# Kernel optimization log

Hardware: AMD Instinct MI355X
Metric: run time of the kernel (lower is better)

The kernel has to match this reference:

```python
import jax, jax.numpy as jnp
import numpy as np

B, S, H = 8, 2048, 256
MAX_SEQ = 2048


def get_rotary_matrix(context_window, embedding_dim):
    # Faithful to the llama-from-scratch construction (note the (i-1) quirk):
    # theta_i = 10000 ** (-2*(i-1)/d) for i in [0, d/2)
    half = embedding_dim // 2
    i = jnp.arange(half, dtype=jnp.float32)
    theta = jnp.power(10000.0, -2.0 * (i - 1.0) / embedding_dim)  # [half]
    pos = jnp.arange(context_window, dtype=jnp.float32)  # [S]
    ang = pos[:, None] * theta[None, :]  # [S, half]
    c, s = jnp.cos(ang), jnp.sin(ang)
    R = jnp.zeros((context_window, embedding_dim, embedding_dim), dtype=jnp.float32)
    idx = jnp.arange(half)
    R = R.at[:, 2 * idx, 2 * idx].set(c)
    R = R.at[:, 2 * idx, 2 * idx + 1].set(-s)
    R = R.at[:, 2 * idx + 1, 2 * idx].set(s)
    R = R.at[:, 2 * idx + 1, 2 * idx + 1].set(c)
    return R


def setup_inputs() -> dict:
    key = jax.random.key(0)
    kx, kq, kk, kv = jax.random.split(key, 4)
    scale = 1.0 / np.sqrt(H)
    x = jax.random.normal(kx, (B, S, H), dtype=jnp.float32)
    wq = jax.random.uniform(kq, (H, H), dtype=jnp.float32, minval=-scale, maxval=scale)
    wk = jax.random.uniform(kk, (H, H), dtype=jnp.float32, minval=-scale, maxval=scale)
    wv = jax.random.uniform(kv, (H, H), dtype=jnp.float32, minval=-scale, maxval=scale)
    r = get_rotary_matrix(MAX_SEQ, H)
    return {"x": x, "wq": wq, "wk": wk, "wv": wv, "r": r}


def reference(x, wq, wk, wv, r):
    b, s, h = x.shape
    # nn.Linear(bias=False): y = x @ W.T
    q = jnp.einsum("bsh,oh->bso", x, wq)
    k = jnp.einsum("bsh,oh->bso", x, wk)
    v = jnp.einsum("bsh,oh->bso", x, wv)
    # per-position dense rotary rotation: qr[b,s,:] = q[b,s,:] @ r[s]
    rs = r[:s]
    qr = jnp.einsum("bsh,shk->bsk", q, rs)
    kr = jnp.einsum("bsh,shk->bsk", k, rs)
    attn = jnp.einsum("bqh,bkh->bqk", qr, kr) * (h ** -0.5)  # [B,S,S]
    causal = jnp.tril(jnp.ones((s, s), dtype=bool))
    attn = jnp.where(causal[None, :, :], attn, -jnp.inf)
    attn = jax.nn.softmax(attn, axis=-1)
    out = jnp.einsum("bqk,bkh->bqh", attn, v)
    return out
```

## Files before the change

### kernel.cpp

```cpp
#include <hip/hip_runtime.h>


typedef __bf16 bf16x8 __attribute__((ext_vector_type(8)));
typedef float  f32x4  __attribute__((ext_vector_type(4)));
typedef unsigned short u16x4 __attribute__((ext_vector_type(4)));

#define LOG2E 1.44269504088896340736f
#define LOG2_10000 13.287712379549449f

__device__ __forceinline__ unsigned short f2bf(float f) {
    union { __bf16 h; unsigned short u; } cv;
    cv.h = (__bf16)f;
    return cv.u;
}

__device__ __forceinline__ void gl_lds16(const unsigned short* g, unsigned short* lds) {
    __builtin_amdgcn_global_load_lds(
        (const __attribute__((address_space(1))) unsigned int*)g,
        (__attribute__((address_space(3))) unsigned int*)lds, 16, 0, 0);
}

__global__ __launch_bounds__(256) void build_cs(float2* __restrict__ cs) {
    int id = blockIdx.x * 256 + threadIdx.x;
    int s = id >> 7;
    int i = id & 127;
    float ex = -2.0f * ((float)i - 1.0f) * (1.0f / 256.0f);
    float theta = exp2f(LOG2_10000 * ex);
    float ang = (float)s * theta;
    float sn, c;
    sincosf(ang, &sn, &c);
    cs[id] = make_float2(c, sn);
}

__global__ __launch_bounds__(256, 2) void qkv_rope(
    const float* __restrict__ x,
    const float* __restrict__ wq, const float* __restrict__ wk,
    const float* __restrict__ wv,
    const float2* __restrict__ cs,
    unsigned short* __restrict__ qr, unsigned short* __restrict__ kr,
    unsigned short* __restrict__ vt) {

    __shared__ unsigned short Ash[64 * 64];
    __shared__ unsigned short Bsh[256 * 64];

    const int mt  = blockIdx.x;
    const int sel = blockIdx.y;
    const float* wsel = (sel == 0) ? wq : (sel == 1) ? wk : wv;

    const int tid = threadIdx.x;
    const int w = tid >> 6, l = tid & 63;
    const int lane_m = l & 15, quad = l >> 4;
    const int wm = w >> 1, wn = w & 1;

    f32x4 acc[2][8];
#pragma unroll
    for (int a = 0; a < 2; ++a)
#pragma unroll
        for (int c = 0; c < 8; ++c) acc[a][c] = (f32x4){0.f, 0.f, 0.f, 0.f};

    for (int kc = 0; kc < 4; ++kc) {
        if (kc) __syncthreads();
#pragma unroll
        for (int p = 0; p < 4; ++p) {
            int id = p * 256 + tid;
            int row = id >> 4, f4 = id & 15;
            float4 d = *(const float4*)(x + (size_t)(mt * 64 + row) * 256 + kc * 64 + f4 * 4);
            u16x4 pk = { f2bf(d.x), f2bf(d.y), f2bf(d.z), f2bf(d.w) };
            int k = f4 * 4;
            int idx = row * 64 + ((((k >> 3) ^ (row & 7)) << 3) | (k & 7));
            *(u16x4*)&Ash[idx] = pk;
        }
#pragma unroll
        for (int p = 0; p < 16; ++p) {
            int id = p * 256 + tid;
            int row = id >> 4, f4 = id & 15;
            float4 d = *(const float4*)(wsel + (size_t)row * 256 + kc * 64 + f4 * 4);
            u16x4 pk = { f2bf(d.x), f2bf(d.y), f2bf(d.z), f2bf(d.w) };
            int k = f4 * 4;
            int idx = row * 64 + ((((k >> 3) ^ (row & 7)) << 3) | (k & 7));
            *(u16x4*)&Bsh[idx] = pk;
        }
        __syncthreads();
#pragma unroll
        for (int ks = 0; ks < 2; ++ks) {
            int ch = ks * 4 + quad;
            int r0 = wm * 32 + lane_m;
            bf16x8 a0 = *(const bf16x8*)&Ash[r0 * 64 + ((ch ^ (r0 & 7)) << 3)];
            bf16x8 a1 = *(const bf16x8*)&Ash[(r0 + 16) * 64 + ((ch ^ (r0 & 7)) << 3)];
#pragma unroll
            for (int ct = 0; ct < 8; ++ct) {
                int n = wn * 128 + ct * 16 + lane_m;
                bf16x8 bb = *(const bf16x8*)&Bsh[n * 64 + ((ch ^ (n & 7)) << 3)];
                acc[0][ct] = __builtin_amdgcn_mfma_f32_16x16x32_bf16(a0, bb, acc[0][ct], 0, 0, 0);
                acc[1][ct] = __builtin_amdgcn_mfma_f32_16x16x32_bf16(a1, bb, acc[1][ct], 0, 0, 0);
            }
        }
    }

    if (sel < 2) {
        unsigned short* dst = sel ? kr : qr;
        const float scale = sel ? 1.0f : 0.0625f;
#pragma unroll
        for (int rt = 0; rt < 2; ++rt) {
#pragma unroll
            for (int ct = 0; ct < 8; ++ct) {
                int col = wn * 128 + ct * 16 + lane_m;
                int ii = col >> 1;
                float sgn = (col & 1) ? -1.0f : 1.0f;
                int mbase = mt * 64 + wm * 32 + rt * 16 + quad * 4;
#pragma unroll
                for (int rr = 0; rr < 4; ++rr) {
                    int m = mbase + rr;
                    int spos = m & 2047;
                    float2 csv = cs[spos * 128 + ii];
                    float v = acc[rt][ct][rr];
                    float pr = __shfl_xor(v, 1);
                    float rot = (csv.x * v + sgn * csv.y * pr) * scale;
                    dst[(size_t)m * 256 + col] = f2bf(rot);
                }
            }
        }
    } else {
#pragma unroll
        for (int rt = 0; rt < 2; ++rt) {
#pragma unroll
            for (int ct = 0; ct < 8; ++ct) {
                int col = wn * 128 + ct * 16 + lane_m;
                int mbase = mt * 64 + wm * 32 + rt * 16 + quad * 4;
                u16x4 pk = { f2bf(acc[rt][ct][0]), f2bf(acc[rt][ct][1]),
                             f2bf(acc[rt][ct][2]), f2bf(acc[rt][ct][3]) };
                int bb = mbase >> 11;
                int s0 = mbase & 2047;
                *(u16x4*)&vt[((size_t)bb * 256 + col) * 2048 + s0] = pk;
            }
        }
    }
}

__global__ __launch_bounds__(256, 2) void flash_attn(
    const unsigned short* __restrict__ qr, const unsigned short* __restrict__ kr,
    const unsigned short* __restrict__ vt, float* __restrict__ out) {

    __shared__ unsigned short Ksh[64 * 256];
    __shared__ unsigned short Vsh[256 * 64];
    __shared__ unsigned short Psh[32 * 64];

    const int n = blockIdx.x;
    const int r = (n < 256) ? n : 767 - n;
    const int b = r & 7;
    const int j = 63 - (r >> 3);
    const int q0 = j * 32;

    const int tid = threadIdx.x;
    const int w = tid >> 6, l = tid & 63;
    const int lane_m = l & 15, quad = l >> 4;
    const int qw = w >> 1;
    const int kp = w & 1;

    bf16x8 qf[8];
    {
        const unsigned short* qb =
            qr + ((size_t)(b * 2048 + q0 + qw * 16 + lane_m)) * 256 + quad * 8;
#pragma unroll
        for (int ks = 0; ks < 8; ++ks) qf[ks] = *(const bf16x8*)(qb + ks * 32);
    }

    f32x4 o[16];
#pragma unroll
    for (int t = 0; t < 16; ++t) o[t] = (f32x4){0.f, 0.f, 0.f, 0.f};
    float l_part[4] = {0.f, 0.f, 0.f, 0.f};

    const int nkt = ((q0 + 31) >> 6) + 1;
    const int rmax = q0 + qw * 16 + 15;

    for (int kt = 0; kt < nkt; ++kt) {
        const int kv0 = kt * 64;
        __syncthreads();
#pragma unroll
        for (int p = 0; p < 8; ++p) {
            int rb = (p * 4 + w) * 2;
            int row = rb + (l >> 5);
            int cg = (l & 31) ^ (row & 31);
            gl_lds16(kr + ((size_t)(b * 2048 + kv0 + row)) * 256 + cg * 8, &Ksh[rb * 256]);
        }
#pragma unroll
        for (int p = 0; p < 8; ++p) {
            int hb = (p * 4 + w) * 8;
            int h = hb + (l >> 3);
            int cg = (l & 7) ^ (h & 7);
            gl_lds16(vt + ((size_t)(b * 256 + h)) * 2048 + kv0 + cg * 8, &Vsh[hb * 64]);
        }
        __syncthreads();

        const bool active = (kv0 + 32 * kp) <= rmax;
        if (active) {
            f32x4 sacc[2];
#pragma unroll
            for (int ct = 0; ct < 2; ++ct) sacc[ct] = (f32x4){0.f, 0.f, 0.f, 0.f};
#pragma unroll
            for (int ks = 0; ks < 8; ++ks) {
                bf16x8 a = qf[ks];
#pragma unroll
                for (int ct = 0; ct < 2; ++ct) {
                    int kvr = kp * 32 + ct * 16 + lane_m;
                    bf16x8 bb = *(const bf16x8*)&Ksh[kvr * 256 + (((ks * 4 + quad) ^ (kvr & 31)) << 3)];
                    sacc[ct] = __builtin_amdgcn_mfma_f32_16x16x32_bf16(a, bb, sacc[ct], 0, 0, 0);
                }
            }

            const bool needmask = (kv0 + kp * 32 + 31) > (q0 + qw * 16);
#pragma unroll
            for (int ct = 0; ct < 2; ++ct) {
                int col_l = kp * 32 + ct * 16 + lane_m;
                int col_g = kv0 + col_l;
#pragma unroll
                for (int rr = 0; rr < 4; ++rr) {
                    float e = exp2f(sacc[ct][rr] * LOG2E);
                    if (needmask) {
                        int row_g = q0 + qw * 16 + quad * 4 + rr;
                        if (col_g > row_g) e = 0.0f;
                    }
                    l_part[rr] += e;
                    int row = qw * 16 + quad * 4 + rr;
                    Psh[row * 64 + ((((col_l >> 3) ^ (row & 7)) << 3) | (col_l & 7))] = f2bf(e);
                }
            }

            {
                int prow = qw * 16 + lane_m;
                int pk = kp * 4 + quad;
                bf16x8 a = *(const bf16x8*)&Psh[prow * 64 + ((pk ^ (prow & 7)) << 3)];
#pragma unroll
                for (int ht = 0; ht < 16; ++ht) {
                    int h = ht * 16 + lane_m;
                    bf16x8 bb = *(const bf16x8*)&Vsh[h * 64 + ((pk ^ (h & 7)) << 3)];
                    o[ht] = __builtin_amdgcn_mfma_f32_16x16x32_bf16(a, bb, o[ht], 0, 0, 0);
                }
            }
        }
    }

#pragma unroll
    for (int rr = 0; rr < 4; ++rr) {
        l_part[rr] += __shfl_xor(l_part[rr], 1);
        l_part[rr] += __shfl_xor(l_part[rr], 2);
        l_part[rr] += __shfl_xor(l_part[rr], 4);
        l_part[rr] += __shfl_xor(l_part[rr], 8);
    }

    __syncthreads();
    float* mlbuf = (float*)Vsh;
    float* obuf  = (float*)Ksh;
    if (lane_m == 0) {
#pragma unroll
        for (int rr = 0; rr < 4; ++rr)
            mlbuf[(qw * 2 + kp) * 16 + quad * 4 + rr] = l_part[rr];
    }
    if (kp == 1) {
#pragma unroll
        for (int ht = 0; ht < 16; ++ht)
#pragma unroll
            for (int rr = 0; rr < 4; ++rr)
                obuf[(qw * 16 + quad * 4 + rr) * 256 + ht * 16 + lane_m] = o[ht][rr];
    }
    __syncthreads();
    if (kp == 0) {
        float inv[4];
#pragma unroll
        for (int rr = 0; rr < 4; ++rr)
            inv[rr] = 1.0f / (l_part[rr] + mlbuf[(qw * 2 + 1) * 16 + quad * 4 + rr]);
#pragma unroll
        for (int ht = 0; ht < 16; ++ht) {
#pragma unroll
            for (int rr = 0; rr < 4; ++rr) {
                float val = o[ht][rr] +
                            obuf[(qw * 16 + quad * 4 + rr) * 256 + ht * 16 + lane_m];
                size_t idx = ((size_t)(b * 2048 + q0 + qw * 16 + quad * 4 + rr)) * 256
                             + ht * 16 + lane_m;
                out[idx] = val * inv[rr];
            }
        }
    }
}

extern "C" void kernel_launch(void* const* d_in, const int* in_sizes, int n_in,
                              void* d_out, int out_size, void* d_ws, size_t ws_size,
                              hipStream_t stream) {
    const float* x  = (const float*)d_in[0];
    const float* wq = (const float*)d_in[1];
    const float* wk = (const float*)d_in[2];
    const float* wv = (const float*)d_in[3];
    float* out = (float*)d_out;

    char* ws = (char*)d_ws;
    float2*         cs = (float2*)ws;
    unsigned short* qr = (unsigned short*)(ws + (2u << 20));
    unsigned short* kr = (unsigned short*)(ws + (10u << 20));
    unsigned short* vt = (unsigned short*)(ws + (18u << 20));

    build_cs<<<dim3(1024), dim3(256), 0, stream>>>(cs);
    qkv_rope<<<dim3(256, 3), dim3(256), 0, stream>>>(x, wq, wk, wv, cs, qr, kr, vt);
    flash_attn<<<dim3(512), dim3(256), 0, stream>>>(qr, kr, vt, out);
}
```

Before: 683.6 us.

## Pre-convert weights to bf16 and compute Q/K/V from one x tile per block

New measurement: 698.7 us. 2.2% more time.

```diff
diff --git a/kernel.cpp b/kernel.cpp
--- a/kernel.cpp
+++ b/kernel.cpp
@@ -20,118 +20,128 @@
         (__attribute__((address_space(3))) unsigned int*)lds, 16, 0, 0);
 }
 
-__global__ __launch_bounds__(256) void build_cs(float2* __restrict__ cs) {
-    int id = blockIdx.x * 256 + threadIdx.x;
-    int s = id >> 7;
-    int i = id & 127;
-    float ex = -2.0f * ((float)i - 1.0f) * (1.0f / 256.0f);
-    float theta = exp2f(LOG2_10000 * ex);
-    float ang = (float)s * theta;
-    float sn, c;
-    sincosf(ang, &sn, &c);
-    cs[id] = make_float2(c, sn);
-}
-
-__global__ __launch_bounds__(256, 2) void qkv_rope(
-    const float* __restrict__ x,
+__global__ __launch_bounds__(256) void prep(
     const float* __restrict__ wq, const float* __restrict__ wk,
     const float* __restrict__ wv,
+    float2* __restrict__ cs, unsigned short* __restrict__ wb) {
+    int bid = blockIdx.x;
+    if (bid < 1024) {
+        int id = bid * 256 + threadIdx.x;
+        int s = id >> 7;
+        int i = id & 127;
+        float ex = -2.0f * ((float)i - 1.0f) * (1.0f / 256.0f);
+        float theta = exp2f(LOG2_10000 * ex);
+        float ang = (float)s * theta;
+        float sn, c;
+        sincosf(ang, &sn, &c);
+        cs[id] = make_float2(c, sn);
+    } else {
+        int id = (bid - 1024) * 256 + threadIdx.x;
+        int sel = id >> 14;
+        int off = id & 16383;
+        const float* src = (sel == 0) ? wq : (sel == 1) ? wk : wv;
+        float4 d = ((const float4*)src)[off];
+        u16x4 pk = { f2bf(d.x), f2bf(d.y), f2bf(d.z), f2bf(d.w) };
+        *(u16x4*)&wb[(size_t)sel * 65536 + (size_t)off * 4] = pk;
+    }
+}
+
+__global__ __launch_bounds__(256, 2) void qkv_rope(
+    const float* __restrict__ x, const unsigned short* __restrict__ wb,
     const float2* __restrict__ cs,
     unsigned short* __restrict__ qr, unsigned short* __restrict__ kr,
     unsigned short* __restrict__ vt) {
 
-    __shared__ unsigned short Ash[64 * 64];
+    __shared__ unsigned short Ash[64 * 256];
     __shared__ unsigned short Bsh[256 * 64];
 
     const int mt  = blockIdx.x;
-    const int sel = blockIdx.y;
-    const float* wsel = (sel == 0) ? wq : (sel == 1) ? wk : wv;
-
     const int tid = threadIdx.x;
     const int w = tid >> 6, l = tid & 63;
     const int lane_m = l & 15, quad = l >> 4;
     const int wm = w >> 1, wn = w & 1;
 
-    f32x4 acc[2][8];
-#pragma unroll
-    for (int a = 0; a < 2; ++a)
-#pragma unroll
-        for (int c = 0; c < 8; ++c) acc[a][c] = (f32x4){0.f, 0.f, 0.f, 0.f};
-
-    for (int kc = 0; kc < 4; ++kc) {
-        if (kc) __syncthreads();
-#pragma unroll
-        for (int p = 0; p < 4; ++p) {
-            int id = p * 256 + tid;
-            int row = id >> 4, f4 = id & 15;
-            float4 d = *(const float4*)(x + (size_t)(mt * 64 + row) * 256 + kc * 64 + f4 * 4);
-            u16x4 pk = { f2bf(d.x), f2bf(d.y), f2bf(d.z), f2bf(d.w) };
-            int k = f4 * 4;
-            int idx = row * 64 + ((((k >> 3) ^ (row & 7)) << 3) | (k & 7));
-            *(u16x4*)&Ash[idx] = pk;
-        }
-#pragma unroll
-        for (int p = 0; p < 16; ++p) {
-            int id = p * 256 + tid;
-            int row = id >> 4, f4 = id & 15;
-            float4 d = *(const float4*)(wsel + (size_t)row * 256 + kc * 64 + f4 * 4);
-            u16x4 pk = { f2bf(d.x), f2bf(d.y), f2bf(d.z), f2bf(d.w) };
-            int k = f4 * 4;
-            int idx = row * 64 + ((((k >> 3) ^ (row & 7)) << 3) | (k & 7));
-            *(u16x4*)&Bsh[idx] = pk;
-        }
-        __syncthreads();
-#pragma unroll
-        for (int ks = 0; ks < 2; ++ks) {
-            int ch = ks * 4 + quad;
-            int r0 = wm * 32 + lane_m;
-            bf16x8 a0 = *(const bf16x8*)&Ash[r0 * 64 + ((ch ^ (r0 & 7)) << 3)];
-            bf16x8 a1 = *(const bf16x8*)&Ash[(r0 + 16) * 64 + ((ch ^ (r0 & 7)) << 3)];
-#pragma unroll
-            for (int ct = 0; ct < 8; ++ct) {
-                int n = wn * 128 + ct * 16 + lane_m;
-                bf16x8 bb = *(const bf16x8*)&Bsh[n * 64 + ((ch ^ (n & 7)) << 3)];
-                acc[0][ct] = __builtin_amdgcn_mfma_f32_16x16x32_bf16(a0, bb, acc[0][ct], 0, 0, 0);
-                acc[1][ct] = __builtin_amdgcn_mfma_f32_16x16x32_bf16(a1, bb, acc[1][ct], 0, 0, 0);
-            }
-        }
-    }
-
-    if (sel < 2) {
-        unsigned short* dst = sel ? kr : qr;
-        const float scale = sel ? 1.0f : 0.0625f;
-#pragma unroll
-        for (int rt = 0; rt < 2; ++rt) {
-#pragma unroll
-            for (int ct = 0; ct < 8; ++ct) {
-                int col = wn * 128 + ct * 16 + lane_m;
-                int ii = col >> 1;
-                float sgn = (col & 1) ? -1.0f : 1.0f;
-                int mbase = mt * 64 + wm * 32 + rt * 16 + quad * 4;
-#pragma unroll
-                for (int rr = 0; rr < 4; ++rr) {
-                    int m = mbase + rr;
-                    int spos = m & 2047;
-                    float2 csv = cs[spos * 128 + ii];
-                    float v = acc[rt][ct][rr];
-                    float pr = __shfl_xor(v, 1);
-                    float rot = (csv.x * v + sgn * csv.y * pr) * scale;
-                    dst[(size_t)m * 256 + col] = f2bf(rot);
-                }
-            }
-        }
-    } else {
-#pragma unroll
-        for (int rt = 0; rt < 2; ++rt) {
-#pragma unroll
-            for (int ct = 0; ct < 8; ++ct) {
-                int col = wn * 128 + ct * 16 + lane_m;
-                int mbase = mt * 64 + wm * 32 + rt * 16 + quad * 4;
-                u16x4 pk = { f2bf(acc[rt][ct][0]), f2bf(acc[rt][ct][1]),
-                             f2bf(acc[rt][ct][2]), f2bf(acc[rt][ct][3]) };
-                int bb = mbase >> 11;
-                int s0 = mbase & 2047;
-                *(u16x4*)&vt[((size_t)bb * 256 + col) * 2048 + s0] = pk;
+#pragma unroll
+    for (int p = 0; p < 16; ++p) {
+        int id = p * 256 + tid;
+        int row = id >> 6, f4 = id & 63;
+        float4 d = *(const float4*)(x + (size_t)(mt * 64 + row) * 256 + f4 * 4);
+        u16x4 pk = { f2bf(d.x), f2bf(d.y), f2bf(d.z), f2bf(d.w) };
+        int k = f4 * 4;
+        int idx = row * 256 + ((((k >> 3) ^ (row & 31)) << 3) | (k & 7));
+        *(u16x4*)&Ash[idx] = pk;
+    }
+
+    for (int sel = 0; sel < 3; ++sel) {
+        f32x4 acc[2][8];
+#pragma unroll
+        for (int a = 0; a < 2; ++a)
+#pragma unroll
+            for (int c = 0; c < 8; ++c) acc[a][c] = (f32x4){0.f, 0.f, 0.f, 0.f};
+
+        for (int kc = 0; kc < 4; ++kc) {
+            __syncthreads();
+#pragma unroll
+            for (int p = 0; p < 8; ++p) {
+                int rb = (p * 4 + w) * 8;
+                int rowg = rb + (l >> 3);
+                int cg = (l & 7) ^ (rowg & 7);
+                gl_lds16(wb + (size_t)sel * 65536 + (size_t)rowg * 256 + kc * 64 + cg * 8,
+                         &Bsh[rb * 64]);
+            }
+            __syncthreads();
+#pragma unroll
+            for (int ks = 0; ks < 2; ++ks) {
+                int ck = kc * 8 + ks * 4 + quad;
+                int r0 = wm * 32 + lane_m, r1 = r0 + 16;
+                bf16x8 a0 = *(const bf16x8*)&Ash[r0 * 256 + ((ck ^ (r0 & 31)) << 3)];
+                bf16x8 a1 = *(const bf16x8*)&Ash[r1 * 256 + ((ck ^ (r1 & 31)) << 3)];
+#pragma unroll
+                for (int ct = 0; ct < 8; ++ct) {
+                    int n = wn * 128 + ct * 16 + lane_m;
+                    bf16x8 bb = *(const bf16x8*)&Bsh[n * 64 + (((ks * 4 + quad) ^ (n & 7)) << 3)];
+                    acc[0][ct] = __builtin_amdgcn_mfma_f32_16x16x32_bf16(a0, bb, acc[0][ct], 0, 0, 0);
+                    acc[1][ct] = __builtin_amdgcn_mfma_f32_16x16x32_bf16(a1, bb, acc[1][ct], 0, 0, 0);
+                }
+            }
+        }
+
+        if (sel < 2) {
+            unsigned short* dst = sel ? kr : qr;
+            const float scale = sel ? 1.0f : 0.0625f;
+#pragma unroll
+            for (int rt = 0; rt < 2; ++rt) {
+#pragma unroll
+                for (int ct = 0; ct < 8; ++ct) {
+                    int col = wn * 128 + ct * 16 + lane_m;
+                    int ii = col >> 1;
+                    float sgn = (col & 1) ? -1.0f : 1.0f;
+                    int mbase = mt * 64 + wm * 32 + rt * 16 + quad * 4;
+#pragma unroll
+                    for (int rr = 0; rr < 4; ++rr) {
+                        int m = mbase + rr;
+                        int spos = m & 2047;
+                        float2 csv = cs[spos * 128 + ii];
+                        float v = acc[rt][ct][rr];
+                        float pr = __shfl_xor(v, 1);
+                        float rot = (csv.x * v + sgn * csv.y * pr) * scale;
+                        dst[(size_t)m * 256 + col] = f2bf(rot);
+                    }
+                }
+            }
+        } else {
+#pragma unroll
+            for (int rt = 0; rt < 2; ++rt) {
+#pragma unroll
+                for (int ct = 0; ct < 8; ++ct) {
+                    int col = wn * 128 + ct * 16 + lane_m;
+                    int mbase = mt * 64 + wm * 32 + rt * 16 + quad * 4;
+                    u16x4 pk = { f2bf(acc[rt][ct][0]), f2bf(acc[rt][ct][1]),
+                                 f2bf(acc[rt][ct][2]), f2bf(acc[rt][ct][3]) };
+                    int bb = mbase >> 11;
+                    int s0 = mbase & 2047;
+                    *(u16x4*)&vt[((size_t)bb * 256 + col) * 2048 + s0] = pk;
+                }
             }
         }
     }
@@ -297,8 +307,9 @@
     unsigned short* qr = (unsigned short*)(ws + (2u << 20));
     unsigned short* kr = (unsigned short*)(ws + (10u << 20));
     unsigned short* vt = (unsigned short*)(ws + (18u << 20));
-
-    build_cs<<<dim3(1024), dim3(256), 0, stream>>>(cs);
-    qkv_rope<<<dim3(256, 3), dim3(256), 0, stream>>>(x, wq, wk, wv, cs, qr, kr, vt);
+    unsigned short* wb = (unsigned short*)(ws + (26u << 20));
+
+    prep<<<dim3(1216), dim3(256), 0, stream>>>(wq, wk, wv, cs, wb);
+    qkv_rope<<<dim3(256), dim3(256), 0, stream>>>(x, wb, cs, qr, kr, vt);
     flash_attn<<<dim3(512), dim3(256), 0, stream>>>(qr, kr, vt, out);
 }
```
